# Kernel optimization log

Measured on AMD Instinct MI355X. Metric: run time of the kernel, lower is better.

The kernel has to match this reference:

```python
import jax, jax.numpy as jnp
import numpy as np

B, F, U, V, C = 2048, 128, 1024, 512, 10

def setup_inputs() -> dict:
    key = jax.random.key(0)
    ks = jax.random.split(key, 8)
    s = lambda k, shape, fan: jax.random.normal(k, shape, dtype=jnp.float32) / np.sqrt(fan)
    return {
        "x": jax.random.normal(ks[0], (B, F), dtype=jnp.float32),
        # ExU first layer per feature: input dim 1 -> U units; weight stored pre-exp
        "exu_w": jax.random.normal(ks[1], (F, U), dtype=jnp.float32) * 0.5 + 4.0,
        "exu_b": jax.random.normal(ks[2], (F,), dtype=jnp.float32) * 0.5,
        # hidden dense per feature: U -> V
        "W1": s(ks[3], (F, U, V), U),
        "b1": jnp.zeros((F, V), dtype=jnp.float32),
        # output dense per feature: V -> C
        "W2": s(ks[4], (F, V, C), V),
        "b2": jnp.zeros((F, C), dtype=jnp.float32),
        # global bias over classes
        "b_out": jnp.zeros((C,), dtype=jnp.float32),
    }

def reference(x, exu_w, exu_b, W1, b1, W2, b2, b_out):
    # ExU unit: h = ReLU-1((x - b) * exp(w)); vectorized over all features at once
    # x: [B,F], exu_w/exu_b: [F,U]/[F] -> h: [B,F,U]
    h = jnp.clip((x - exu_b[None, :])[:, :, None] * jnp.exp(exu_w)[None], 0.0, 1.0)
    # grouped hidden GEMM per feature: [B,F,U] x [F,U,V] -> [B,F,V]
    h2 = jax.nn.relu(jnp.einsum('bfu,fuv->bfv', h, W1) + b1[None])
    # grouped output GEMM: [B,F,V] x [F,V,C] -> [B,F,C]
    weights = jnp.einsum('bfv,fvc->bfc', h2, W2) + b2[None]
    # sum feature contributions + bias, softmax over classes (inference, no dropout)
    logits = jnp.sum(weights, axis=1) + b_out
    return jax.nn.softmax(logits, axis=-1)
```

## Files before the change

### kernel.cpp

```cpp
#include <hip/hip_runtime.h>


#define F_ 128
#define U_ 1024
#define V_ 512
#define C_ 10
#define B_ 2048
#define UN 16

__global__ void nam_sort(const float* __restrict__ exu_w, const float* __restrict__ b2,
                         const float* __restrict__ b_out,
                         unsigned long long* __restrict__ skeys_g,
                         float* __restrict__ emin, float* __restrict__ biasc,
                         int* __restrict__ count, float* __restrict__ logits_mid)
{
  const int bid = blockIdx.x, t = threadIdx.x;
  if (bid < F_) {
    __shared__ unsigned long long keys[1024];
    for (int i = t; i < U_; i += 256) {
      float e = expf(exu_w[(size_t)bid * U_ + i]);
      keys[i] = ((unsigned long long)__builtin_bit_cast(unsigned, e) << 32) | (unsigned)i;
    }
    __syncthreads();
    for (int k = 2; k <= 1024; k <<= 1)
      for (int j = k >> 1; j > 0; j >>= 1) {
        for (int i = t; i < 1024; i += 256) {
          const int p = i ^ j;
          if (p > i) {
            unsigned long long a = keys[i], b = keys[p];
            const bool up = ((i & k) == 0);
            if (up ? (a > b) : (a < b)) { keys[i] = b; keys[p] = a; }
          }
        }
        __syncthreads();
      }
    for (int i = t; i < 1024; i += 256) skeys_g[(size_t)bid * U_ + i] = keys[i];
    if (t == 0) emin[bid] = __builtin_bit_cast(float, (unsigned)(keys[0] >> 32));
  } else if (bid == F_) {
    if (t < C_) {
      float s = b_out[t];
      for (int ff = 0; ff < F_; ++ff) s += b2[ff * C_ + t];
      biasc[t] = s;
    } else if (t >= 32 && t < 32 + F_) {
      count[t - 32] = 0;
    }
  } else {
    const int idx = (bid - F_ - 1) * 256 + t;
    logits_mid[idx] = 0.f;
  }
}

__global__ void nam_classify(const float* __restrict__ x, const float* __restrict__ exu_b,
                             const float* __restrict__ emin,
                             int* __restrict__ count, int* __restrict__ listb)
{
  const int t = threadIdx.x;
  const int f = t & 127, sub = t >> 7;
  const int b = blockIdx.x * 2 + sub;
  const float d = x[(size_t)b * F_ + f] - exu_b[f];
  if (d > 0.f && d * emin[f] < 1.f) {
    const int idx = atomicAdd(count + f, 1);
    listb[f * B_ + idx] = b;
  }
}

__global__ __launch_bounds__(128) void nam_stream(
    const float* __restrict__ x, const float* __restrict__ exu_b,
    const float* __restrict__ W1,
    const unsigned long long* __restrict__ skeys_g,
    const int* __restrict__ listb, const int* __restrict__ count,
    float* __restrict__ colsum1, float* __restrict__ h2pre,
    int* __restrict__ bout)
{
  __shared__ unsigned long long skeys[1024];
  __shared__ unsigned pkey[2048];
  __shared__ float    darr[2048];
  __shared__ int      barr[2048];

  const int bx   = blockIdx.x;
  const int f    = bx >> 1;
  const int half = bx & 1;
  const int tid  = threadIdx.x;

  for (int i = tid; i < 1024; i += 128) skeys[i] = skeys_g[(size_t)f * U_ + i];
  const int nmid = count[f];
  const float bfv = exu_b[f];
  __syncthreads();

  for (int i = tid; i < nmid; i += 128) {
    const int b = listb[f * B_ + i];
    const float d = x[(size_t)b * F_ + f] - bfv;
    darr[i] = d;
    barr[i] = b;
    const float thr = 1.0f / d;
    int lo = 0, hi = 1024;
#pragma unroll
    for (int s = 0; s < 10; ++s) {
      const int mid = (lo + hi) >> 1;
      const float e = __builtin_bit_cast(float, (unsigned)(skeys[mid] >> 32));
      if (e < thr) lo = mid + 1; else hi = mid;
      if (lo >= hi) {  }
    }
    pkey[i] = ((unsigned)lo << 11) | (unsigned)i;
  }
  int npow2 = 2;
  while (npow2 < nmid) npow2 <<= 1;
  for (int i = tid; i < npow2; i += 128)
    if (i >= nmid) pkey[i] = 0xFFFFFFFFu;
  __syncthreads();
  if (nmid > 1) {
    for (int k = 2; k <= npow2; k <<= 1)
      for (int j = k >> 1; j > 0; j >>= 1) {
        for (int i = tid; i < npow2; i += 128) {
          const int p = i ^ j;
          if (p > i) {
            unsigned a = pkey[i], b = pkey[p];
            const bool up = ((i & k) == 0);
            if (up ? (a > b) : (a < b)) { pkey[i] = b; pkey[p] = a; }
          }
        }
        __syncthreads();
      }
  }

  const float* Wf = W1 + (size_t)f * (U_ * V_) + half * 256 + 2 * tid;
  typedef __attribute__((ext_vector_type(2))) float f2;
  f2 cur[UN], nxt[UN];
  float ecur[UN], enxt[UN];
#pragma unroll
  for (int q = 0; q < UN; ++q) {
    const unsigned long long kk = skeys[q];
    cur[q] = *(const f2*)(Wf + ((unsigned)(kk & 1023u) << 9));
    ecur[q] = __builtin_bit_cast(float, (unsigned)(kk >> 32));
  }
  float S0 = 0.f, S1 = 0.f, T0 = 0.f, T1 = 0.f;
  int pp = 0;
  int next_r = (nmid > 0) ? (int)(pkey[0] >> 11) : 99999;

  for (int blk = 0; blk < 1024 / UN; ++blk) {
    if (blk < 1024 / UN - 1) {
#pragma unroll
      for (int q = 0; q < UN; ++q) {
        const unsigned long long kk = skeys[(blk + 1) * UN + q];
        nxt[q] = *(const f2*)(Wf + ((unsigned)(kk & 1023u) << 9));
        enxt[q] = __builtin_bit_cast(float, (unsigned)(kk >> 32));
      }
    }
#pragma unroll
    for (int q = 0; q < UN; ++q) {
      const int i = blk * UN + q;
      while (pp < nmid && next_r <= i) {
        const unsigned pk = pkey[pp];
        const int idx = (int)(pk & 2047u);
        const float dd = darr[idx];
        f2 outv;
        outv.x = dd * S0 - T0;
        outv.y = dd * S1 - T1;
        *(f2*)(h2pre + ((size_t)f * B_ + pp) * V_ + half * 256 + 2 * tid) = outv;
        if (tid == 0 && half == 0) bout[f * B_ + pp] = barr[idx];
        ++pp;
        next_r = (pp < nmid) ? (int)(pkey[pp] >> 11) : 99999;
      }
      const float e = ecur[q];
      const f2 wv = cur[q];
      S0 = fmaf(e, wv.x, S0);
      S1 = fmaf(e, wv.y, S1);
      T0 += wv.x;
      T1 += wv.y;
    }
#pragma unroll
    for (int q = 0; q < UN; ++q) { cur[q] = nxt[q]; ecur[q] = enxt[q]; }
  }
  while (pp < nmid) {
    const unsigned pk = pkey[pp];
    const int idx = (int)(pk & 2047u);
    const float dd = darr[idx];
    f2 outv;
    outv.x = dd * S0 - T0;
    outv.y = dd * S1 - T1;
    *(f2*)(h2pre + ((size_t)f * B_ + pp) * V_ + half * 256 + 2 * tid) = outv;
    if (tid == 0 && half == 0) bout[f * B_ + pp] = barr[idx];
    ++pp;
  }
  f2 cs; cs.x = T0; cs.y = T1;
  *(f2*)(colsum1 + f * V_ + half * 256 + 2 * tid) = cs;
}

__global__ void nam_fin_mid(const int* __restrict__ count, const int* __restrict__ bout,
                            const float* __restrict__ h2pre, const float* __restrict__ colsum1,
                            const float* __restrict__ b1, const float* __restrict__ W2,
                            float* __restrict__ logits_mid)
{
  const int f = blockIdx.x, t = threadIdx.x;
  const int wave = t >> 6, lane = t & 63;
  const int nmid = count[f];
  for (int row = wave; row < nmid; row += 4) {
    const int b = bout[f * B_ + row];
    const float* pre = h2pre + ((size_t)f * B_ + row) * V_ + lane * 8;
    const float* csp = colsum1 + f * V_ + lane * 8;
    const float* b1p = b1 + (size_t)f * V_ + lane * 8;
    float acc[C_];
#pragma unroll
    for (int c = 0; c < C_; ++c) acc[c] = 0.f;
#pragma unroll
    for (int j = 0; j < 8; ++j) {
      const float h = fmaxf(pre[j] + csp[j] + b1p[j], 0.f);
      const float* w2p = W2 + ((size_t)f * V_ + lane * 8 + j) * C_;
#pragma unroll
      for (int c = 0; c < C_; ++c) acc[c] = fmaf(h, w2p[c], acc[c]);
    }
#pragma unroll
    for (int off = 32; off > 0; off >>= 1)
#pragma unroll
      for (int c = 0; c < C_; ++c) acc[c] += __shfl_down(acc[c], off);
    if (lane == 0)
#pragma unroll
      for (int c = 0; c < C_; ++c) atomicAdd(logits_mid + (size_t)b * C_ + c, acc[c]);
  }
}

__global__ void nam_tables(const float* __restrict__ colsum1, const float* __restrict__ b1,
                           const float* __restrict__ W2,
                           float* __restrict__ zlog, float* __restrict__ olog)
{
  const int f = blockIdx.x, t = threadIdx.x;
  float a0[C_], a1[C_];
#pragma unroll
  for (int c = 0; c < C_; ++c) { a0[c] = 0.f; a1[c] = 0.f; }
#pragma unroll
  for (int rep = 0; rep < 2; ++rep) {
    const int v = t + rep * 256;
    const float b1v = b1[(size_t)f * V_ + v];
    const float hz = fmaxf(b1v, 0.f);
    const float ho = fmaxf(colsum1[(size_t)f * V_ + v] + b1v, 0.f);
    const float* w2p = W2 + ((size_t)f * V_ + v) * C_;
#pragma unroll
    for (int c = 0; c < C_; ++c) {
      const float wv = w2p[c];
      a0[c] += hz * wv;
      a1[c] += ho * wv;
    }
  }
#pragma unroll
  for (int off = 32; off > 0; off >>= 1)
#pragma unroll
    for (int c = 0; c < C_; ++c) {
      a0[c] += __shfl_down(a0[c], off);
      a1[c] += __shfl_down(a1[c], off);
    }
  __shared__ float red[4][2 * C_];
  const int wv_ = t >> 6, ln = t & 63;
  if (ln == 0)
#pragma unroll
    for (int c = 0; c < C_; ++c) { red[wv_][c] = a0[c]; red[wv_][C_ + c] = a1[c]; }
  __syncthreads();
  if (t < 2 * C_) {
    const float s = red[0][t] + red[1][t] + red[2][t] + red[3][t];
    if (t < C_) zlog[t * F_ + f] = s;
    else        olog[(t - C_) * F_ + f] = s;
  }
}

__global__ void nam_final(const float* __restrict__ x, const float* __restrict__ exu_b,
                          const float* __restrict__ emin,
                          const float* __restrict__ zlog, const float* __restrict__ olog,
                          const float* __restrict__ biasc, const float* __restrict__ logits_mid,
                          float* __restrict__ out)
{
  const int t = threadIdx.x;
  const int f = t & 127, sub = t >> 7;
  const int b = blockIdx.x * 2 + sub;
  const float d  = x[(size_t)b * F_ + f] - exu_b[f];
  const float em = emin[f];
  const bool is_zero = !(d > 0.f);
  const bool is_one  = (d > 0.f) && (d * em >= 1.f);
  float a[C_];
#pragma unroll
  for (int c = 0; c < C_; ++c) {
    const float zv = zlog[c * F_ + f];
    const float ov = olog[c * F_ + f];
    a[c] = is_zero ? zv : (is_one ? ov : 0.f);
  }
#pragma unroll
  for (int off = 32; off > 0; off >>= 1)
#pragma unroll
    for (int c = 0; c < C_; ++c) a[c] += __shfl_down(a[c], off);
  __shared__ float red[4][C_];
  __shared__ float lg[2][C_];
  const int wv_ = t >> 6, ln = t & 63;
  if (ln == 0)
#pragma unroll
    for (int c = 0; c < C_; ++c) red[wv_][c] = a[c];
  __syncthreads();
  if (t < 2 * C_) {
    const int rb = t / C_, c = t % C_;
    lg[rb][c] = red[rb * 2][c] + red[rb * 2 + 1][c]
              + logits_mid[(size_t)(blockIdx.x * 2 + rb) * C_ + c] + biasc[c];
  }
  __syncthreads();
  if (t < 2) {
    float mx = -3.0e38f;
#pragma unroll
    for (int c = 0; c < C_; ++c) mx = fmaxf(mx, lg[t][c]);
    float e[C_];
    float s = 0.f;
#pragma unroll
    for (int c = 0; c < C_; ++c) { e[c] = expf(lg[t][c] - mx); s += e[c]; }
    const float inv = 1.f / s;
#pragma unroll
    for (int c = 0; c < C_; ++c) out[(size_t)(blockIdx.x * 2 + t) * C_ + c] = e[c] * inv;
  }
}

extern "C" void kernel_launch(void* const* d_in, const int* in_sizes, int n_in,
                              void* d_out, int out_size, void* d_ws, size_t ws_size,
                              hipStream_t stream)
{
  const float* x     = (const float*)d_in[0];
  const float* exu_w = (const float*)d_in[1];
  const float* exu_b = (const float*)d_in[2];
  const float* W1    = (const float*)d_in[3];
  const float* b1    = (const float*)d_in[4];
  const float* W2    = (const float*)d_in[5];
  const float* b2    = (const float*)d_in[6];
  const float* b_out = (const float*)d_in[7];
  float* out = (float*)d_out;

  char* ws = (char*)d_ws;
  float* emin       = (float*)(ws + 0);
  float* biasc      = (float*)(ws + 512);
  int*   count      = (int*)  (ws + 576);
  int*   listb      = (int*)  (ws + 1088);
  float* colsum1    = (float*)(ws + 1049664);
  float* zlog       = (float*)(ws + 1311808);
  float* olog       = (float*)(ws + 1316928);
  float* logits_mid = (float*)(ws + 1322048);
  unsigned long long* skeys_g = (unsigned long long*)(ws + 1404928);
  int*   bout       = (int*)  (ws + 2453504);
  float* h2pre      = (float*)(ws + 4194304);

  nam_sort<<<F_ + 1 + (B_ * C_ / 256), 256, 0, stream>>>(exu_w, b2, b_out, skeys_g,
                                                          emin, biasc, count, logits_mid);
  nam_classify<<<B_ / 2, 256, 0, stream>>>(x, exu_b, emin, count, listb);
  nam_stream<<<F_ * 2, 128, 0, stream>>>(x, exu_b, W1, skeys_g, listb, count,
                                          colsum1, h2pre, bout);
  nam_fin_mid<<<F_, 256, 0, stream>>>(count, bout, h2pre, colsum1, b1, W2, logits_mid);
  nam_tables<<<F_, 256, 0, stream>>>(colsum1, b1, W2, zlog, olog);
  nam_final<<<B_ / 2, 256, 0, stream>>>(x, exu_b, emin, zlog, olog, biasc, logits_mid, out);
}
```

Measured before the change: 515.7 us.

## Split W1 streaming across U-slices per feature and fuse fin_mid with tables

The W1 streaming kernel now splits each feature's sorted U range into 8 slices of 128, giving 1024 blocks of 256 threads instead of 256 blocks of 128. Each slice writes partial S/T sums. A merged finishing kernel prefix-sums the slices and corrects each mid-row's partial h2pre with d*S-T for the preceding slices. The nam_tables kernel is folded into this finisher, removing one launch. The aim is to use more of the GPU and cut the serial 1024-step stream per block. The cost is more workspace, redundant binary searches in every slice, and extra per-row metadata (rank, d).

```diff
diff --git a/kernel.cpp b/kernel.cpp
--- a/kernel.cpp
+++ b/kernel.cpp
@@ -6,7 +6,16 @@
 #define V_ 512
 #define C_ 10
 #define B_ 2048
+#define NSL 8
+#define SLW 128
 #define UN 16
+
+typedef __attribute__((ext_vector_type(2))) float f2;
+typedef __attribute__((ext_vector_type(4))) float fx4;
+
+__device__ __forceinline__ float ebits(unsigned long long k) {
+  return __builtin_bit_cast(float, (unsigned)(k >> 32));
+}
 
 __global__ void nam_sort(const float* __restrict__ exu_w, const float* __restrict__ b2,
                          const float* __restrict__ b_out,
@@ -35,7 +44,7 @@
         __syncthreads();
       }
     for (int i = t; i < 1024; i += 256) skeys_g[(size_t)bid * U_ + i] = keys[i];
-    if (t == 0) emin[bid] = __builtin_bit_cast(float, (unsigned)(keys[0] >> 32));
+    if (t == 0) emin[bid] = ebits(keys[0]);
   } else if (bid == F_) {
     if (t < C_) {
       float s = b_out[t];
@@ -64,54 +73,54 @@
   }
 }
 
-__global__ __launch_bounds__(128) void nam_stream(
+__global__ __launch_bounds__(256) void nam_stream2(
     const float* __restrict__ x, const float* __restrict__ exu_b,
     const float* __restrict__ W1,
     const unsigned long long* __restrict__ skeys_g,
     const int* __restrict__ listb, const int* __restrict__ count,
-    float* __restrict__ colsum1, float* __restrict__ h2pre,
-    int* __restrict__ bout)
+    float* __restrict__ sliceS, float* __restrict__ sliceT,
+    float* __restrict__ h2pre, int* __restrict__ rnk,
+    float* __restrict__ ddv, int* __restrict__ bout)
 {
   __shared__ unsigned long long skeys[1024];
   __shared__ unsigned pkey[2048];
-  __shared__ float    darr[2048];
-  __shared__ int      barr[2048];
-
-  const int bx   = blockIdx.x;
-  const int f    = bx >> 1;
-  const int half = bx & 1;
-  const int tid  = threadIdx.x;
-
-  for (int i = tid; i < 1024; i += 128) skeys[i] = skeys_g[(size_t)f * U_ + i];
+  __shared__ int cnt_s;
+
+  const int f   = blockIdx.x >> 3;
+  const int sl  = blockIdx.x & 7;
+  const int tid = threadIdx.x;
+
+  for (int i = tid; i < 1024; i += 256) skeys[i] = skeys_g[(size_t)f * U_ + i];
+  if (tid == 0) cnt_s = 0;
   const int nmid = count[f];
   const float bfv = exu_b[f];
   __syncthreads();
 
-  for (int i = tid; i < nmid; i += 128) {
+  for (int i = tid; i < nmid; i += 256) {
     const int b = listb[f * B_ + i];
     const float d = x[(size_t)b * F_ + f] - bfv;
-    darr[i] = d;
-    barr[i] = b;
     const float thr = 1.0f / d;
     int lo = 0, hi = 1024;
-#pragma unroll
-    for (int s = 0; s < 10; ++s) {
+    while (lo < hi) {
       const int mid = (lo + hi) >> 1;
-      const float e = __builtin_bit_cast(float, (unsigned)(skeys[mid] >> 32));
-      if (e < thr) lo = mid + 1; else hi = mid;
-      if (lo >= hi) {  }
-    }
-    pkey[i] = ((unsigned)lo << 11) | (unsigned)i;
-  }
-  int npow2 = 2;
-  while (npow2 < nmid) npow2 <<= 1;
-  for (int i = tid; i < npow2; i += 128)
-    if (i >= nmid) pkey[i] = 0xFFFFFFFFu;
-  __syncthreads();
-  if (nmid > 1) {
+      if (ebits(skeys[mid]) < thr) lo = mid + 1; else hi = mid;
+    }
+    int s_of = lo >> 7; if (s_of > 7) s_of = 7;
+    if (s_of == sl) {
+      const int pos = atomicAdd(&cnt_s, 1);
+      pkey[pos] = ((unsigned)(lo - sl * SLW) << 12) | (unsigned)i;
+    }
+  }
+  __syncthreads();
+  const int cnt = cnt_s;
+  int npow2 = 1; while (npow2 < cnt) npow2 <<= 1; if (npow2 < 2) npow2 = 2;
+  for (int i = tid; i < npow2; i += 256)
+    if (i >= cnt) pkey[i] = 0xFFFFFFFFu;
+  __syncthreads();
+  if (cnt > 1) {
     for (int k = 2; k <= npow2; k <<= 1)
       for (int j = k >> 1; j > 0; j >>= 1) {
-        for (int i = tid; i < npow2; i += 128) {
+        for (int i = tid; i < npow2; i += 256) {
           const int p = i ^ j;
           if (p > i) {
             unsigned a = pkey[i], b = pkey[p];
@@ -123,44 +132,50 @@
       }
   }
 
-  const float* Wf = W1 + (size_t)f * (U_ * V_) + half * 256 + 2 * tid;
-  typedef __attribute__((ext_vector_type(2))) float f2;
+  const float* Wf = W1 + (size_t)f * (U_ * V_) + 2 * tid;
+  const int kb = sl * SLW;
   f2 cur[UN], nxt[UN];
   float ecur[UN], enxt[UN];
 #pragma unroll
   for (int q = 0; q < UN; ++q) {
-    const unsigned long long kk = skeys[q];
-    cur[q] = *(const f2*)(Wf + ((unsigned)(kk & 1023u) << 9));
-    ecur[q] = __builtin_bit_cast(float, (unsigned)(kk >> 32));
+    const unsigned long long kk = skeys[kb + q];
+    cur[q] = *(const f2*)(Wf + ((size_t)(unsigned)(kk & 1023u) << 9));
+    ecur[q] = ebits(kk);
   }
   float S0 = 0.f, S1 = 0.f, T0 = 0.f, T1 = 0.f;
   int pp = 0;
-  int next_r = (nmid > 0) ? (int)(pkey[0] >> 11) : 99999;
-
-  for (int blk = 0; blk < 1024 / UN; ++blk) {
-    if (blk < 1024 / UN - 1) {
+  int next_rl = (cnt > 0) ? (int)(pkey[0] >> 12) : (1 << 20);
+
+#define EMIT()                                                                   \
+  {                                                                              \
+    const unsigned pk = pkey[pp];                                                \
+    const int li = (int)(pk & 0xFFFu);                                           \
+    const int bb = listb[f * B_ + li];                                           \
+    const float dd = x[(size_t)bb * F_ + f] - bfv;                               \
+    f2 o; o.x = dd * S0 - T0; o.y = dd * S1 - T1;                                \
+    *(f2*)(h2pre + (size_t)(f * B_ + li) * V_ + 2 * tid) = o;                    \
+    if (tid == 0) {                                                              \
+      bout[f * B_ + li] = bb;                                                    \
+      ddv[f * B_ + li]  = dd;                                                    \
+      rnk[f * B_ + li]  = kb + (int)(pk >> 12);                                  \
+    }                                                                            \
+    ++pp;                                                                        \
+    next_rl = (pp < cnt) ? (int)(pkey[pp] >> 12) : (1 << 20);                    \
+  }
+
+  for (int blk = 0; blk < SLW / UN; ++blk) {
+    if (blk < SLW / UN - 1) {
 #pragma unroll
       for (int q = 0; q < UN; ++q) {
-        const unsigned long long kk = skeys[(blk + 1) * UN + q];
-        nxt[q] = *(const f2*)(Wf + ((unsigned)(kk & 1023u) << 9));
-        enxt[q] = __builtin_bit_cast(float, (unsigned)(kk >> 32));
+        const unsigned long long kk = skeys[kb + (blk + 1) * UN + q];
+        nxt[q] = *(const f2*)(Wf + ((size_t)(unsigned)(kk & 1023u) << 9));
+        enxt[q] = ebits(kk);
       }
     }
 #pragma unroll
     for (int q = 0; q < UN; ++q) {
-      const int i = blk * UN + q;
-      while (pp < nmid && next_r <= i) {
-        const unsigned pk = pkey[pp];
-        const int idx = (int)(pk & 2047u);
-        const float dd = darr[idx];
-        f2 outv;
-        outv.x = dd * S0 - T0;
-        outv.y = dd * S1 - T1;
-        *(f2*)(h2pre + ((size_t)f * B_ + pp) * V_ + half * 256 + 2 * tid) = outv;
-        if (tid == 0 && half == 0) bout[f * B_ + pp] = barr[idx];
-        ++pp;
-        next_r = (pp < nmid) ? (int)(pkey[pp] >> 11) : 99999;
-      }
+      const int j = blk * UN + q;
+      while (pp < cnt && next_rl <= j) EMIT();
       const float e = ecur[q];
       const f2 wv = cur[q];
       S0 = fmaf(e, wv.x, S0);
@@ -171,74 +186,58 @@
 #pragma unroll
     for (int q = 0; q < UN; ++q) { cur[q] = nxt[q]; ecur[q] = enxt[q]; }
   }
-  while (pp < nmid) {
-    const unsigned pk = pkey[pp];
-    const int idx = (int)(pk & 2047u);
-    const float dd = darr[idx];
-    f2 outv;
-    outv.x = dd * S0 - T0;
-    outv.y = dd * S1 - T1;
-    *(f2*)(h2pre + ((size_t)f * B_ + pp) * V_ + half * 256 + 2 * tid) = outv;
-    if (tid == 0 && half == 0) bout[f * B_ + pp] = barr[idx];
-    ++pp;
-  }
-  f2 cs; cs.x = T0; cs.y = T1;
-  *(f2*)(colsum1 + f * V_ + half * 256 + 2 * tid) = cs;
-}
-
-__global__ void nam_fin_mid(const int* __restrict__ count, const int* __restrict__ bout,
-                            const float* __restrict__ h2pre, const float* __restrict__ colsum1,
-                            const float* __restrict__ b1, const float* __restrict__ W2,
-                            float* __restrict__ logits_mid)
-{
-  const int f = blockIdx.x, t = threadIdx.x;
-  const int wave = t >> 6, lane = t & 63;
-  const int nmid = count[f];
-  for (int row = wave; row < nmid; row += 4) {
-    const int b = bout[f * B_ + row];
-    const float* pre = h2pre + ((size_t)f * B_ + row) * V_ + lane * 8;
-    const float* csp = colsum1 + f * V_ + lane * 8;
-    const float* b1p = b1 + (size_t)f * V_ + lane * 8;
-    float acc[C_];
-#pragma unroll
-    for (int c = 0; c < C_; ++c) acc[c] = 0.f;
-#pragma unroll
-    for (int j = 0; j < 8; ++j) {
-      const float h = fmaxf(pre[j] + csp[j] + b1p[j], 0.f);
-      const float* w2p = W2 + ((size_t)f * V_ + lane * 8 + j) * C_;
-#pragma unroll
-      for (int c = 0; c < C_; ++c) acc[c] = fmaf(h, w2p[c], acc[c]);
-    }
-#pragma unroll
-    for (int off = 32; off > 0; off >>= 1)
-#pragma unroll
-      for (int c = 0; c < C_; ++c) acc[c] += __shfl_down(acc[c], off);
-    if (lane == 0)
-#pragma unroll
-      for (int c = 0; c < C_; ++c) atomicAdd(logits_mid + (size_t)b * C_ + c, acc[c]);
-  }
-}
-
-__global__ void nam_tables(const float* __restrict__ colsum1, const float* __restrict__ b1,
-                           const float* __restrict__ W2,
-                           float* __restrict__ zlog, float* __restrict__ olog)
-{
-  const int f = blockIdx.x, t = threadIdx.x;
+  while (pp < cnt) EMIT();
+#undef EMIT
+
+  {
+    f2 sv; sv.x = S0; sv.y = S1;
+    f2 tv; tv.x = T0; tv.y = T1;
+    *(f2*)(sliceS + (size_t)(f * NSL + sl) * V_ + 2 * tid) = sv;
+    *(f2*)(sliceT + (size_t)(f * NSL + sl) * V_ + 2 * tid) = tv;
+  }
+}
+
+__global__ __launch_bounds__(256) void nam_finmid(
+    const int* __restrict__ count, const int* __restrict__ rnk,
+    const float* __restrict__ ddv, const int* __restrict__ bout,
+    const float* __restrict__ h2pre,
+    const float* __restrict__ sliceS, const float* __restrict__ sliceT,
+    const float* __restrict__ b1, const float* __restrict__ W2,
+    float* __restrict__ zlog, float* __restrict__ olog,
+    float* __restrict__ logits_mid)
+{
+  __shared__ float Sx[NSL * V_];
+  __shared__ float Tx[NSL * V_];
+  __shared__ float CB[V_];
+  __shared__ float red[4][2 * C_];
+
+  const int f = blockIdx.x, tid = threadIdx.x;
+  const int wave = tid >> 6, lane = tid & 63;
+
   float a0[C_], a1[C_];
 #pragma unroll
   for (int c = 0; c < C_; ++c) { a0[c] = 0.f; a1[c] = 0.f; }
 #pragma unroll
-  for (int rep = 0; rep < 2; ++rep) {
-    const int v = t + rep * 256;
+  for (int k = 0; k < 2; ++k) {
+    const int v = 2 * tid + k;
+    float accS = 0.f, accT = 0.f;
+#pragma unroll
+    for (int s = 0; s < NSL; ++s) {
+      Sx[s * V_ + v] = accS;
+      Tx[s * V_ + v] = accT;
+      accS += sliceS[(size_t)(f * NSL + s) * V_ + v];
+      accT += sliceT[(size_t)(f * NSL + s) * V_ + v];
+    }
     const float b1v = b1[(size_t)f * V_ + v];
+    CB[v] = accT + b1v;
     const float hz = fmaxf(b1v, 0.f);
-    const float ho = fmaxf(colsum1[(size_t)f * V_ + v] + b1v, 0.f);
+    const float ho = fmaxf(accT + b1v, 0.f);
     const float* w2p = W2 + ((size_t)f * V_ + v) * C_;
 #pragma unroll
     for (int c = 0; c < C_; ++c) {
       const float wv = w2p[c];
-      a0[c] += hz * wv;
-      a1[c] += ho * wv;
+      a0[c] = fmaf(hz, wv, a0[c]);
+      a1[c] = fmaf(ho, wv, a1[c]);
     }
   }
 #pragma unroll
@@ -248,16 +247,41 @@
       a0[c] += __shfl_down(a0[c], off);
       a1[c] += __shfl_down(a1[c], off);
     }
-  __shared__ float red[4][2 * C_];
-  const int wv_ = t >> 6, ln = t & 63;
-  if (ln == 0)
-#pragma unroll
-    for (int c = 0; c < C_; ++c) { red[wv_][c] = a0[c]; red[wv_][C_ + c] = a1[c]; }
-  __syncthreads();
-  if (t < 2 * C_) {
-    const float s = red[0][t] + red[1][t] + red[2][t] + red[3][t];
-    if (t < C_) zlog[t * F_ + f] = s;
-    else        olog[(t - C_) * F_ + f] = s;
+  if (lane == 0)
+#pragma unroll
+    for (int c = 0; c < C_; ++c) { red[wave][c] = a0[c]; red[wave][C_ + c] = a1[c]; }
+  __syncthreads();
+  if (tid < 2 * C_) {
+    const float s = red[0][tid] + red[1][tid] + red[2][tid] + red[3][tid];
+    if (tid < C_) zlog[tid * F_ + f] = s;
+    else          olog[(tid - C_) * F_ + f] = s;
+  }
+
+  const int nmid = count[f];
+  for (int row = wave; row < nmid; row += 4) {
+    const float d = ddv[f * B_ + row];
+    const int   r = rnk[f * B_ + row];
+    const int   b = bout[f * B_ + row];
+    int s = r >> 7; if (s > 7) s = 7;
+    const float* pre = h2pre + (size_t)(f * B_ + row) * V_;
+    float acc[C_];
+#pragma unroll
+    for (int c = 0; c < C_; ++c) acc[c] = 0.f;
+#pragma unroll
+    for (int j = 0; j < 8; ++j) {
+      const int v = lane + 64 * j;
+      const float h = fmaxf(pre[v] + d * Sx[s * V_ + v] - Tx[s * V_ + v] + CB[v], 0.f);
+      const float* w2p = W2 + ((size_t)f * V_ + v) * C_;
+#pragma unroll
+      for (int c = 0; c < C_; ++c) acc[c] = fmaf(h, w2p[c], acc[c]);
+    }
+#pragma unroll
+    for (int off = 32; off > 0; off >>= 1)
+#pragma unroll
+      for (int c = 0; c < C_; ++c) acc[c] += __shfl_down(acc[c], off);
+    if (lane == 0)
+#pragma unroll
+      for (int c = 0; c < C_; ++c) atomicAdd(logits_mid + (size_t)b * C_ + c, acc[c]);
   }
 }
 
@@ -329,22 +353,25 @@
   char* ws = (char*)d_ws;
   float* emin       = (float*)(ws + 0);
   float* biasc      = (float*)(ws + 512);
-  int*   count      = (int*)  (ws + 576);
-  int*   listb      = (int*)  (ws + 1088);
-  float* colsum1    = (float*)(ws + 1049664);
-  float* zlog       = (float*)(ws + 1311808);
-  float* olog       = (float*)(ws + 1316928);
-  float* logits_mid = (float*)(ws + 1322048);
-  unsigned long long* skeys_g = (unsigned long long*)(ws + 1404928);
-  int*   bout       = (int*)  (ws + 2453504);
-  float* h2pre      = (float*)(ws + 4194304);
+  int*   count      = (int*)  (ws + 1024);
+  int*   listb      = (int*)  (ws + 2048);
+  float* sliceS     = (float*)(ws + 1050624);
+  float* sliceT     = (float*)(ws + 3147776);
+  float* zlog       = (float*)(ws + 5244928);
+  float* olog       = (float*)(ws + 5250048);
+  float* logits_mid = (float*)(ws + 5255168);
+  unsigned long long* skeys_g = (unsigned long long*)(ws + 5337088);
+  int*   rnk        = (int*)  (ws + 6385664);
+  float* ddv        = (float*)(ws + 7434240);
+  int*   bout       = (int*)  (ws + 8482816);
+  float* h2pre      = (float*)(ws + 16777216);
 
   nam_sort<<<F_ + 1 + (B_ * C_ / 256), 256, 0, stream>>>(exu_w, b2, b_out, skeys_g,
                                                           emin, biasc, count, logits_mid);
   nam_classify<<<B_ / 2, 256, 0, stream>>>(x, exu_b, emin, count, listb);
-  nam_stream<<<F_ * 2, 128, 0, stream>>>(x, exu_b, W1, skeys_g, listb, count,
-                                          colsum1, h2pre, bout);
-  nam_fin_mid<<<F_, 256, 0, stream>>>(count, bout, h2pre, colsum1, b1, W2, logits_mid);
-  nam_tables<<<F_, 256, 0, stream>>>(colsum1, b1, W2, zlog, olog);
+  nam_stream2<<<F_ * NSL, 256, 0, stream>>>(x, exu_b, W1, skeys_g, listb, count,
+                                             sliceS, sliceT, h2pre, rnk, ddv, bout);
+  nam_finmid<<<F_, 256, 0, stream>>>(count, rnk, ddv, bout, h2pre, sliceS, sliceT,
+                                      b1, W2, zlog, olog, logits_mid);
   nam_final<<<B_ / 2, 256, 0, stream>>>(x, exu_b, emin, zlog, olog, biasc, logits_mid, out);
 }
```

New measurement: 532.6 us. 1.03x slower.
